# Kernel optimization log

Hardware: AMD Instinct MI355X
Metric: run time of the kernel (lower is better)

The kernel has to match this reference:

```python
import jax, jax.numpy as jnp
import numpy as np

N_NODES = 100000
N_EDGES = 1600000
IN_DIM, HID_DIM, OUT_DIM = 64, 128, 64


def setup_inputs() -> dict:
    key = jax.random.key(0)
    ks = jax.random.split(key, 12)
    s = 0.02
    x = jax.random.normal(ks[0], (N_NODES, IN_DIM), dtype=jnp.float32)
    edge_index = jax.random.randint(ks[1], (2, N_EDGES), 0, N_NODES, dtype=jnp.int64)
    return {
        "x": x,
        "edge_index": edge_index,
        # SAGEConv layer 1: lin_l (neighbors, with bias), lin_r (root, no bias)
        "w1l": jax.random.normal(ks[2], (HID_DIM, IN_DIM), dtype=jnp.float32) * s,
        "b1l": jnp.zeros((HID_DIM,), dtype=jnp.float32),
        "w1r": jax.random.normal(ks[3], (HID_DIM, IN_DIM), dtype=jnp.float32) * s,
        # SAGEConv layer 2
        "w2l": jax.random.normal(ks[4], (OUT_DIM, HID_DIM), dtype=jnp.float32) * s,
        "b2l": jnp.zeros((OUT_DIM,), dtype=jnp.float32),
        "w2r": jax.random.normal(ks[5], (OUT_DIM, HID_DIM), dtype=jnp.float32) * s,
        # classifier MLP: Linear(128,64) -> ReLU -> Linear(64,2) (dropout off in eval)
        "wc1": jax.random.normal(ks[6], (64, 2 * OUT_DIM), dtype=jnp.float32) * s,
        "bc1": jnp.zeros((64,), dtype=jnp.float32),
        "wc2": jax.random.normal(ks[7], (2, 64), dtype=jnp.float32) * s,
        "bc2": jnp.zeros((2,), dtype=jnp.float32),
    }


def _sage_conv(x, src, dst, wl, bl, wr):
    # PyG SAGEConv (aggr='mean'): out = lin_l(mean_{j in N(i)} x_j) + lin_r(x_i)
    msg = x[src]                                                  # [E, d] gather
    agg = jax.ops.segment_sum(msg, dst, num_segments=N_NODES)     # [N, d] scatter-add
    cnt = jax.ops.segment_sum(jnp.ones((src.shape[0],), x.dtype), dst, num_segments=N_NODES)
    mean = agg / jnp.maximum(cnt, 1.0)[:, None]
    return mean @ wl.T + bl + x @ wr.T


def reference(x, edge_index, w1l, b1l, w1r, w2l, b2l, w2r, wc1, bc1, wc2, bc2):
    src, dst = edge_index[0], edge_index[1]
    h = jax.nn.relu(_sage_conv(x, src, dst, w1l, b1l, w1r))   # dropout: eval mode (identity)
    h = jax.nn.relu(_sage_conv(h, src, dst, w2l, b2l, w2r))
    edge_repr = jnp.concatenate([h[src], h[dst]], axis=1)      # [E, 2*OUT_DIM]
    hidden = jax.nn.relu(edge_repr @ wc1.T + bc1)
    return hidden @ wc2.T + bc2                                 # [E, 2]
```

## Files before the change

kernel.cpp:

```cpp
#include <hip/hip_runtime.h>

#define N_NODES 100000
#define N_EDGES 1600000
#define NBLK_SCAN 391
#define SLICE_NODES 12500
#define BCAP 800000

typedef unsigned int uint;
typedef unsigned short ushort;
typedef __attribute__((ext_vector_type(8))) short bf16x8;
typedef __attribute__((ext_vector_type(4))) float f32x4;

__device__ inline float bflo(uint u) { union { uint i; float f; } c; c.i = u << 16; return c.f; }
__device__ inline float bfhi(uint u) { union { uint i; float f; } c; c.i = u & 0xffff0000u; return c.f; }
__device__ inline float bf2f(ushort h) { union { uint i; float f; } c; c.i = (uint)h << 16; return c.f; }
__device__ inline ushort f2bf(float f) {
    union { float f; uint u; } c; c.f = f;
    uint r = (c.u + 0x7fffu + ((c.u >> 16) & 1u)) >> 16;
    return (ushort)r;
}

#define W1_OFF   0
#define W2L_OFF  16384
#define W2R_OFF  24576
#define WC1_OFF  32768
#define W_TOTAL  40960

__global__ __launch_bounds__(256) void prep_weights(const float* __restrict__ w1r,
                                                    const float* __restrict__ w1l,
                                                    const float* __restrict__ w2l,
                                                    const float* __restrict__ w2r,
                                                    const float* __restrict__ wc1,
                                                    ushort* __restrict__ Whi,
                                                    ushort* __restrict__ Wlo) {
    int idx = blockIdx.x * 256 + threadIdx.x;
    if (idx >= W_TOTAL) return;
    float v;
    if (idx < W2L_OFF) {
        int o = idx >> 7, k = idx & 127;
        v = (k < 64) ? w1r[o * 64 + k] : w1l[o * 64 + (k - 64)];
    } else if (idx < W2R_OFF) {
        int t2 = idx - W2L_OFF; int o = t2 >> 7, k = t2 & 127;
        v = w2l[o * 128 + k];
    } else if (idx < WC1_OFF) {
        int t2 = idx - W2R_OFF; int o = t2 >> 7, k = t2 & 127;
        v = w2r[o * 128 + k];
    } else {
        int t2 = idx - WC1_OFF; int o = t2 >> 6, k = t2 & 63;
        v = wc1[(o & 63) * 128 + ((o >> 6) << 6) + k];
    }
    ushort hi = f2bf(v);
    ushort lo = f2bf(v - bf2f(hi));
    Whi[idx] = hi; Wlo[idx] = lo;
}

__global__ __launch_bounds__(256) void convert_kernel(const float* __restrict__ x,
                                                      ushort* __restrict__ xb) {
    int i = blockIdx.x * 256 + threadIdx.x;
    if (i < N_NODES * 32) {
        float2 v = ((const float2*)x)[i];
        uint o = (uint)f2bf(v.x) | ((uint)f2bf(v.y) << 16);
        ((uint*)xb)[i] = o;
    }
}

__global__ __launch_bounds__(256) void bucket_kernel(const int* __restrict__ src,
                                                     const int* __restrict__ dst,
                                                     int* __restrict__ cnt,
                                                     int* __restrict__ bcur,
                                                     uint* __restrict__ bkt) {
    __shared__ int hist[8];
    __shared__ int bbase[8];
    const int t = threadIdx.x;
    int e = blockIdx.x * 256 + t;
    if (t < 8) hist[t] = 0;
    __syncthreads();
    int b = -1, mo = 0; uint pack = 0;
    if (e < N_EDGES) {
        int d = dst[e], s = src[e];
        atomicAdd(&cnt[d], 1);
        b = d / SLICE_NODES;
        pack = ((uint)(d - b * SLICE_NODES) << 17) | (uint)s;
        mo = atomicAdd(&hist[b], 1);
    }
    __syncthreads();
    if (t < 8) bbase[t] = hist[t] ? atomicAdd(&bcur[t], hist[t]) : 0;
    __syncthreads();
    if (b >= 0) {
        int pos = bbase[b] + mo;
        if (pos < BCAP) bkt[(size_t)b * BCAP + pos] = pack;
    }
}

__global__ __launch_bounds__(256) void scan_block_sums(const int* __restrict__ cnt,
                                                       int* __restrict__ partial) {
    __shared__ int red[4];
    int i = blockIdx.x * 256 + threadIdx.x;
    int v = (i < N_NODES) ? cnt[i] : 0;
#pragma unroll
    for (int off = 32; off; off >>= 1) v += __shfl_down(v, off, 64);
    if ((threadIdx.x & 63) == 0) red[threadIdx.x >> 6] = v;
    __syncthreads();
    if (threadIdx.x == 0) partial[blockIdx.x] = red[0] + red[1] + red[2] + red[3];
}

__global__ __launch_bounds__(512) void scan_top(int* __restrict__ partial) {
    __shared__ int s[512];
    int t = threadIdx.x;
    int orig = (t < NBLK_SCAN) ? partial[t] : 0;
    s[t] = orig;
    __syncthreads();
#pragma unroll
    for (int off = 1; off < 512; off <<= 1) {
        int v = (t >= off) ? s[t - off] : 0;
        __syncthreads();
        s[t] += v;
        __syncthreads();
    }
    if (t < NBLK_SCAN) partial[t] = s[t] - orig;
}

__global__ __launch_bounds__(256) void scan_final(const int* __restrict__ cnt,
                                                  const int* __restrict__ partial,
                                                  int* __restrict__ row_start,
                                                  int* __restrict__ cursor) {
    __shared__ int s[256];
    int i = blockIdx.x * 256 + threadIdx.x;
    int t = threadIdx.x;
    int orig = (i < N_NODES) ? cnt[i] : 0;
    s[t] = orig;
    __syncthreads();
#pragma unroll
    for (int off = 1; off < 256; off <<= 1) {
        int v = (t >= off) ? s[t - off] : 0;
        __syncthreads();
        s[t] += v;
        __syncthreads();
    }
    if (i < N_NODES) {
        int rs = partial[blockIdx.x] + s[t] - orig;
        row_start[i] = rs;
        cursor[i] = rs;
    }
}

__global__ __launch_bounds__(256) void fill_bucketed(const uint* __restrict__ bkt,
                                                     const int* __restrict__ bcur,
                                                     int* __restrict__ cursor,
                                                     int* __restrict__ nbr) {
    int slice = blockIdx.x & 7;
    int chunk = blockIdx.x >> 3;
    int count = min(bcur[slice], BCAP);
    int per = (count + 127) >> 7;
    int start = chunk * per;
    int end = min(start + per, count);
    const uint* B = bkt + (size_t)slice * BCAP;
    for (int i = start + threadIdx.x; i < end; i += 256) {
        uint p = B[i];
        int d = slice * SLICE_NODES + (int)(p >> 17);
        int pos = atomicAdd(&cursor[d], 1);
        nbr[pos] = (int)(p & 0x1FFFFu);
    }
}

__global__ __launch_bounds__(256) void agg_mean64_bf16(const int* __restrict__ row_start,
                                                       const int* __restrict__ cnt,
                                                       const int* __restrict__ nbr,
                                                       const ushort* __restrict__ feat,
                                                       float* __restrict__ outmean) {
    int node = blockIdx.x * 4 + (threadIdx.x >> 6);
    if (node >= N_NODES) return;
    int lane = threadIdx.x & 63;
    int half = lane >> 5;
    int f2   = lane & 31;
    int s = row_start[node];
    int d = cnt[node];
    float ax = 0.0f, ay = 0.0f;
    int p = 0;
    for (; p + 4 <= d; p += 4) {
        int n0 = nbr[s + p + half];
        int n1 = nbr[s + p + 2 + half];
        uint w0 = *(const uint*)(feat + (size_t)n0 * 64 + f2 * 2);
        uint w1 = *(const uint*)(feat + (size_t)n1 * 64 + f2 * 2);
        ax += bflo(w0) + bflo(w1);
        ay += bfhi(w0) + bfhi(w1);
    }
    for (; p + 2 <= d; p += 2) {
        int n0 = nbr[s + p + half];
        uint w0 = *(const uint*)(feat + (size_t)n0 * 64 + f2 * 2);
        ax += bflo(w0);
        ay += bfhi(w0);
    }
    if (p < d && half == 0) {
        int n0 = nbr[s + p];
        uint w0 = *(const uint*)(feat + (size_t)n0 * 64 + f2 * 2);
        ax += bflo(w0);
        ay += bfhi(w0);
    }
    ax += __shfl_xor(ax, 32, 64);
    ay += __shfl_xor(ay, 32, 64);
    if (half == 0) {
        float inv = 1.0f / fmaxf((float)d, 1.0f);
        float2 o; o.x = ax * inv; o.y = ay * inv;
        *(float2*)&outmean[(size_t)node * 64 + f2 * 2] = o;
    }
}

#define MFMA __builtin_amdgcn_mfma_f32_16x16x32_bf16

__global__ __launch_bounds__(256) void g1g2_kernel(const float* __restrict__ x,
                                                   const float* __restrict__ mean1,
                                                   const ushort* __restrict__ Whi,
                                                   const ushort* __restrict__ Wlo,
                                                   const float* __restrict__ b1l,
                                                   ushort* __restrict__ h1hi,
                                                   ushort* __restrict__ y2b) {
    __shared__ ushort Ah[64 * 136];
    __shared__ ushort Al[64 * 136];
    const int t = threadIdx.x;
    const int l = t & 63;
    const int wv = t >> 6;
    const int base = blockIdx.x * 64;
    const int lr = l & 15;
    const int lk = (l >> 4) * 8;

    for (int idx = t; idx < 2048; idx += 256) {
        int halfsel = idx >> 10;
        int id2 = idx & 1023;
        int n = id2 >> 4;
        int k0 = (id2 & 15) * 4;
        int gn = base + n;
        float4 v = make_float4(0.f, 0.f, 0.f, 0.f);
        if (gn < N_NODES) v = *(const float4*)&(halfsel ? mean1 : x)[(size_t)gn * 64 + k0];
        ushort h0 = f2bf(v.x), h1_ = f2bf(v.y), h2_ = f2bf(v.z), h3 = f2bf(v.w);
        ushort l0 = f2bf(v.x - bf2f(h0)), l1 = f2bf(v.y - bf2f(h1_));
        ushort l2 = f2bf(v.z - bf2f(h2_)), l3 = f2bf(v.w - bf2f(h3));
        int col = halfsel * 64 + k0;
        uint2 ph; ph.x = (uint)h0 | ((uint)h1_ << 16); ph.y = (uint)h2_ | ((uint)h3 << 16);
        uint2 pl; pl.x = (uint)l0 | ((uint)l1 << 16); pl.y = (uint)l2 | ((uint)l3 << 16);
        *(uint2*)&Ah[n * 136 + col] = ph;
        *(uint2*)&Al[n * 136 + col] = pl;
    }
    __syncthreads();

    f32x4 acc[4][2];
#pragma unroll
    for (int m4 = 0; m4 < 4; ++m4)
#pragma unroll
        for (int n2 = 0; n2 < 2; ++n2) acc[m4][n2] = (f32x4){0.f, 0.f, 0.f, 0.f};

#pragma unroll
    for (int ks = 0; ks < 4; ++ks) {
        bf16x8 ah[4], al[4];
        int aoff = lr * 136 + ks * 32 + lk;
#pragma unroll
        for (int m4 = 0; m4 < 4; ++m4) {
            ah[m4] = *(const bf16x8*)&Ah[m4 * 2176 + aoff];
            al[m4] = *(const bf16x8*)&Al[m4 * 2176 + aoff];
        }
#pragma unroll
        for (int n2 = 0; n2 < 2; ++n2) {
            int o = wv * 32 + n2 * 16 + lr;
            int woff = W1_OFF + o * 128 + ks * 32 + lk;
            bf16x8 bh = *(const bf16x8*)&Whi[woff];
            bf16x8 bl = *(const bf16x8*)&Wlo[woff];
#pragma unroll
            for (int m4 = 0; m4 < 4; ++m4) {
                acc[m4][n2] = MFMA(al[m4], bh, acc[m4][n2], 0, 0, 0);
                acc[m4][n2] = MFMA(ah[m4], bl, acc[m4][n2], 0, 0, 0);
                acc[m4][n2] = MFMA(ah[m4], bh, acc[m4][n2], 0, 0, 0);
            }
        }
    }
    __syncthreads();
    ushort* H1h = Ah;
    ushort* H1l = Al;

#pragma unroll
    for (int n2 = 0; n2 < 2; ++n2) {
        int o = wv * 32 + n2 * 16 + lr;
        float bb = b1l[o];
#pragma unroll
        for (int m4 = 0; m4 < 4; ++m4) {
#pragma unroll
            for (int r = 0; r < 4; ++r) {
                int nl = m4 * 16 + (l >> 4) * 4 + r;
                float val = fmaxf(acc[m4][n2][r] + bb, 0.f);
                ushort hi = f2bf(val);
                ushort lo = f2bf(val - bf2f(hi));
                H1h[nl * 136 + o] = hi;
                H1l[nl * 136 + o] = lo;
            }
        }
    }
    __syncthreads();

    for (int idx = t; idx < 2048; idx += 256) {
        int n = idx >> 5;
        int c4 = (idx & 31) * 4;
        int gn = base + n;
        if (gn < N_NODES)
            *(uint2*)&h1hi[(size_t)gn * 128 + c4] = *(uint2*)&H1h[n * 136 + c4];
    }

    f32x4 acc2[4];
#pragma unroll
    for (int m4 = 0; m4 < 4; ++m4) acc2[m4] = (f32x4){0.f, 0.f, 0.f, 0.f};
#pragma unroll
    for (int ks = 0; ks < 4; ++ks) {
        int aoff = lr * 136 + ks * 32 + lk;
        int o2 = wv * 16 + lr;
        int woff = W2L_OFF + o2 * 128 + ks * 32 + lk;
        bf16x8 bh = *(const bf16x8*)&Whi[woff];
        bf16x8 bl = *(const bf16x8*)&Wlo[woff];
#pragma unroll
        for (int m4 = 0; m4 < 4; ++m4) {
            bf16x8 ah = *(const bf16x8*)&H1h[m4 * 2176 + aoff];
            bf16x8 al = *(const bf16x8*)&H1l[m4 * 2176 + aoff];
            acc2[m4] = MFMA(al, bh, acc2[m4], 0, 0, 0);
            acc2[m4] = MFMA(ah, bl, acc2[m4], 0, 0, 0);
            acc2[m4] = MFMA(ah, bh, acc2[m4], 0, 0, 0);
        }
    }
#pragma unroll
    for (int m4 = 0; m4 < 4; ++m4) {
#pragma unroll
        for (int r = 0; r < 4; ++r) {
            int nl = m4 * 16 + (l >> 4) * 4 + r;
            int gn = base + nl;
            if (gn < N_NODES) y2b[(size_t)gn * 64 + wv * 16 + lr] = f2bf(acc2[m4][r]);
        }
    }
}

__global__ __launch_bounds__(256) void g3g4_kernel(const ushort* __restrict__ h1hi,
                                                   const float* __restrict__ mean2,
                                                   const ushort* __restrict__ Whi,
                                                   const ushort* __restrict__ Wlo,
                                                   const float* __restrict__ b2l,
                                                   const float* __restrict__ bc1,
                                                   ushort* __restrict__ uvb) {
    __shared__ ushort H1h[64 * 136];
    __shared__ float  M2[64 * 68];
    __shared__ ushort H2l[64 * 72];
    const int t = threadIdx.x;
    const int l = t & 63;
    const int wv = t >> 6;
    const int base = blockIdx.x * 64;
    const int lr = l & 15;
    const int lk = (l >> 4) * 8;

    for (int idx = t; idx < 2048; idx += 256) {
        int n = idx >> 5;
        int c4 = (idx & 31) * 4;
        int gn = base + n;
        uint2 vh = make_uint2(0u, 0u);
        if (gn < N_NODES) vh = *(const uint2*)&h1hi[(size_t)gn * 128 + c4];
        *(uint2*)&H1h[n * 136 + c4] = vh;
    }
    for (int idx = t; idx < 1024; idx += 256) {
        int n = idx >> 4;
        int k0 = (idx & 15) * 4;
        int gn = base + n;
        float4 v = make_float4(0.f, 0.f, 0.f, 0.f);
        if (gn < N_NODES) v = *(const float4*)&mean2[(size_t)gn * 64 + k0];
        *(float4*)&M2[n * 68 + k0] = v;
    }
    __syncthreads();

    f32x4 acc[4];
#pragma unroll
    for (int m4 = 0; m4 < 4; ++m4) acc[m4] = (f32x4){0.f, 0.f, 0.f, 0.f};
#pragma unroll
    for (int ks = 0; ks < 4; ++ks) {
        int aoff = lr * 136 + ks * 32 + lk;
        int o2 = wv * 16 + lr;
        int woff = W2R_OFF + o2 * 128 + ks * 32 + lk;
        bf16x8 bh = *(const bf16x8*)&Whi[woff];
        bf16x8 bl = *(const bf16x8*)&Wlo[woff];
#pragma unroll
        for (int m4 = 0; m4 < 4; ++m4) {
            bf16x8 ah = *(const bf16x8*)&H1h[m4 * 2176 + aoff];
            acc[m4] = MFMA(ah, bl, acc[m4], 0, 0, 0);
            acc[m4] = MFMA(ah, bh, acc[m4], 0, 0, 0);
        }
    }
    __syncthreads();
    ushort* H2h = H1h;

    {
        int o2 = wv * 16 + lr;
        float bb = b2l[o2];
#pragma unroll
        for (int m4 = 0; m4 < 4; ++m4) {
#pragma unroll
            for (int r = 0; r < 4; ++r) {
                int nl = m4 * 16 + (l >> 4) * 4 + r;
                float val = fmaxf(acc[m4][r] + M2[nl * 68 + o2] + bb, 0.f);
                ushort hi = f2bf(val);
                ushort lo = f2bf(val - bf2f(hi));
                H2h[nl * 72 + o2] = hi;
                H2l[nl * 72 + o2] = lo;
            }
        }
    }
    __syncthreads();

    f32x4 acc4[4][2];
#pragma unroll
    for (int m4 = 0; m4 < 4; ++m4)
#pragma unroll
        for (int n2 = 0; n2 < 2; ++n2) acc4[m4][n2] = (f32x4){0.f, 0.f, 0.f, 0.f};
#pragma unroll
    for (int ks = 0; ks < 2; ++ks) {
        bf16x8 ah[4], al[4];
        int aoff = lr * 72 + ks * 32 + lk;
#pragma unroll
        for (int m4 = 0; m4 < 4; ++m4) {
            ah[m4] = *(const bf16x8*)&H2h[m4 * 1152 + aoff];
            al[m4] = *(const bf16x8*)&H2l[m4 * 1152 + aoff];
        }
#pragma unroll
        for (int n2 = 0; n2 < 2; ++n2) {
            int o = wv * 32 + n2 * 16 + lr;
            int woff = WC1_OFF + o * 64 + ks * 32 + lk;
            bf16x8 bh = *(const bf16x8*)&Whi[woff];
            bf16x8 bl = *(const bf16x8*)&Wlo[woff];
#pragma unroll
            for (int m4 = 0; m4 < 4; ++m4) {
                acc4[m4][n2] = MFMA(al[m4], bh, acc4[m4][n2], 0, 0, 0);
                acc4[m4][n2] = MFMA(ah[m4], bl, acc4[m4][n2], 0, 0, 0);
                acc4[m4][n2] = MFMA(ah[m4], bh, acc4[m4][n2], 0, 0, 0);
            }
        }
    }
#pragma unroll
    for (int n2 = 0; n2 < 2; ++n2) {
        int o = wv * 32 + n2 * 16 + lr;
        float bb = (o < 64) ? bc1[o] : 0.0f;
#pragma unroll
        for (int m4 = 0; m4 < 4; ++m4) {
#pragma unroll
            for (int r = 0; r < 4; ++r) {
                int nl = m4 * 16 + (l >> 4) * 4 + r;
                int gn = base + nl;
                if (gn < N_NODES) uvb[(size_t)gn * 128 + o] = f2bf(acc4[m4][n2][r] + bb);
            }
        }
    }
}

__global__ __launch_bounds__(256) void edge_kernel(const int* __restrict__ src,
                                                   const int* __restrict__ dst,
                                                   const ushort* __restrict__ uvb,
                                                   const float* __restrict__ wc2,
                                                   const float* __restrict__ bc2,
                                                   float* __restrict__ out) {
    int e = blockIdx.x * blockDim.x + threadIdx.x;
    if (e >= N_EDGES) return;
    const uint4* ua = (const uint4*)(uvb + (size_t)src[e] * 128);
    const uint4* va = (const uint4*)(uvb + (size_t)dst[e] * 128 + 64);
    float o0 = 0.0f, o1 = 0.0f;
#pragma unroll
    for (int k = 0; k < 8; ++k) {
        uint4 a = ua[k], b = va[k];
        int i0 = k * 8;
        float h0, h1v;
        h0 = fmaxf(bflo(a.x) + bflo(b.x), 0.f); h1v = fmaxf(bfhi(a.x) + bfhi(b.x), 0.f);
        o0 += wc2[i0] * h0 + wc2[i0 + 1] * h1v;  o1 += wc2[64 + i0] * h0 + wc2[65 + i0] * h1v;
        h0 = fmaxf(bflo(a.y) + bflo(b.y), 0.f); h1v = fmaxf(bfhi(a.y) + bfhi(b.y), 0.f);
        o0 += wc2[i0 + 2] * h0 + wc2[i0 + 3] * h1v;  o1 += wc2[66 + i0] * h0 + wc2[67 + i0] * h1v;
        h0 = fmaxf(bflo(a.z) + bflo(b.z), 0.f); h1v = fmaxf(bfhi(a.z) + bfhi(b.z), 0.f);
        o0 += wc2[i0 + 4] * h0 + wc2[i0 + 5] * h1v;  o1 += wc2[68 + i0] * h0 + wc2[69 + i0] * h1v;
        h0 = fmaxf(bflo(a.w) + bflo(b.w), 0.f); h1v = fmaxf(bfhi(a.w) + bfhi(b.w), 0.f);
        o0 += wc2[i0 + 6] * h0 + wc2[i0 + 7] * h1v;  o1 += wc2[70 + i0] * h0 + wc2[71 + i0] * h1v;
    }
    float2 r;
    r.x = o0 + bc2[0];
    r.y = o1 + bc2[1];
    *(float2*)(out + (size_t)e * 2) = r;
}

extern "C" void kernel_launch(void* const* d_in, const int* in_sizes, int n_in,
                              void* d_out, int out_size, void* d_ws, size_t ws_size,
                              hipStream_t stream) {
    const float* x   = (const float*)d_in[0];
    const int*   ei  = (const int*)d_in[1];
    const float* w1l = (const float*)d_in[2];
    const float* b1l = (const float*)d_in[3];
    const float* w1r = (const float*)d_in[4];
    const float* w2l = (const float*)d_in[5];
    const float* b2l = (const float*)d_in[6];
    const float* w2r = (const float*)d_in[7];
    const float* wc1 = (const float*)d_in[8];
    const float* bc1 = (const float*)d_in[9];
    const float* wc2 = (const float*)d_in[10];
    const float* bc2 = (const float*)d_in[11];
    float* out = (float*)d_out;

    const int* srcp = ei;
    const int* dstp = ei + N_EDGES;

    float*  ws    = (float*)d_ws;
    ushort* xb    = (ushort*)ws;
    ushort* y2b   = (ushort*)ws;
    float*  mean1 = ws + 3200000;
    ushort* uvb   = (ushort*)(ws + 3200000);
    ushort* h1hi  = (ushort*)(ws + 9600000);
    uint*   bkt   = (uint*)(ws + 16000000);
    float*  mean2 = ws + 22400000;
    int*    ib    = (int*)(ws + 28800000);
    int* cnt       = ib;
    int* row_start = ib + 100000;
    int* cursor    = ib + 200000;
    int* partial   = ib + 300000;
    int* bcur      = ib + 300512;
    int* nbr       = ib + 300520;
    ushort* Whi = (ushort*)(ws + 30800000);
    ushort* Wlo = (ushort*)(ws + 30900000);

    hipMemsetAsync(cnt, 0, (size_t)N_NODES * 4, stream);
    hipMemsetAsync(bcur, 0, 8 * 4, stream);

    prep_weights<<<(W_TOTAL + 255) / 256, 256, 0, stream>>>(w1r, w1l, w2l, w2r, wc1, Whi, Wlo);
    convert_kernel<<<12500, 256, 0, stream>>>(x, xb);

    bucket_kernel<<<(N_EDGES + 255) / 256, 256, 0, stream>>>(srcp, dstp, cnt, bcur, bkt);
    scan_block_sums<<<NBLK_SCAN, 256, 0, stream>>>(cnt, partial);
    scan_top<<<1, 512, 0, stream>>>(partial);
    scan_final<<<NBLK_SCAN, 256, 0, stream>>>(cnt, partial, row_start, cursor);
    fill_bucketed<<<1024, 256, 0, stream>>>(bkt, bcur, cursor, nbr);

    const int NAB = (N_NODES + 3) / 4;
    const int NB  = (N_NODES + 63) / 64;

    agg_mean64_bf16<<<NAB, 256, 0, stream>>>(row_start, cnt, nbr, xb, mean1);
    g1g2_kernel<<<NB, 256, 0, stream>>>(x, mean1, Whi, Wlo, b1l, h1hi, y2b);
    agg_mean64_bf16<<<NAB, 256, 0, stream>>>(row_start, cnt, nbr, y2b, mean2);
    g3g4_kernel<<<NB, 256, 0, stream>>>(h1hi, mean2, Whi, Wlo, b2l, bc1, uvb);
    edge_kernel<<<(N_EDGES + 255) / 256, 256, 0, stream>>>(srcp, dstp, uvb, wc2, bc2, out);
}
```

Measured before the change: 470.9 us.

## Split bucket counters into 64 groups and process 2048 edges per block

The bucketing kernel now gives each block 2048 edges instead of 256. It counts slice histograms in a first pass and scatters in a second pass. Blocks are spread over 8 groups of bucket counters (64 counters in total), which cuts global-atomic contention on the 8 shared bucket cursors. The fill kernel is reorganised to walk the 64 sub-buckets. The cost is that dst is read twice and each sub-bucket has a cap of 100000, which the uniform random input should stay under.

```diff
diff --git a/kernel.cpp b/kernel.cpp
--- a/kernel.cpp
+++ b/kernel.cpp
@@ -4,7 +4,9 @@
 #define N_EDGES 1600000
 #define NBLK_SCAN 391
 #define SLICE_NODES 12500
-#define BCAP 800000
+#define BCAP 100000
+#define EPB 2048
+#define NBLK_BKT 782
 
 typedef unsigned int uint;
 typedef unsigned short ushort;
@@ -69,26 +71,28 @@
                                                      int* __restrict__ cnt,
                                                      int* __restrict__ bcur,
                                                      uint* __restrict__ bkt) {
-    __shared__ int hist[8];
-    __shared__ int bbase[8];
+    __shared__ int hist[8], hist2[8], bbase[8];
     const int t = threadIdx.x;
-    int e = blockIdx.x * 256 + t;
-    if (t < 8) hist[t] = 0;
-    __syncthreads();
-    int b = -1, mo = 0; uint pack = 0;
-    if (e < N_EDGES) {
+    const int g = blockIdx.x & 7;
+    const int ebase = blockIdx.x * EPB;
+    const int eend = min(ebase + EPB, N_EDGES);
+    if (t < 8) { hist[t] = 0; hist2[t] = 0; }
+    __syncthreads();
+    for (int e = ebase + t; e < eend; e += 256) {
+        int d = dst[e];
+        atomicAdd(&cnt[d], 1);
+        atomicAdd(&hist[d / SLICE_NODES], 1);
+    }
+    __syncthreads();
+    if (t < 8) bbase[t] = hist[t] ? atomicAdd(&bcur[g * 8 + t], hist[t]) : 0;
+    __syncthreads();
+    for (int e = ebase + t; e < eend; e += 256) {
         int d = dst[e], s = src[e];
-        atomicAdd(&cnt[d], 1);
-        b = d / SLICE_NODES;
-        pack = ((uint)(d - b * SLICE_NODES) << 17) | (uint)s;
-        mo = atomicAdd(&hist[b], 1);
-    }
-    __syncthreads();
-    if (t < 8) bbase[t] = hist[t] ? atomicAdd(&bcur[t], hist[t]) : 0;
-    __syncthreads();
-    if (b >= 0) {
+        int b = d / SLICE_NODES;
+        uint pack = ((uint)(d - b * SLICE_NODES) << 17) | (uint)s;
+        int mo = atomicAdd(&hist2[b], 1);
         int pos = bbase[b] + mo;
-        if (pos < BCAP) bkt[(size_t)b * BCAP + pos] = pack;
+        if (pos < BCAP) bkt[(size_t)(g * 8 + b) * BCAP + pos] = pack;
     }
 }
 
@@ -148,16 +152,17 @@
                                                      const int* __restrict__ bcur,
                                                      int* __restrict__ cursor,
                                                      int* __restrict__ nbr) {
-    int slice = blockIdx.x & 7;
-    int chunk = blockIdx.x >> 3;
-    int count = min(bcur[slice], BCAP);
-    int per = (count + 127) >> 7;
+    int s = blockIdx.x & 7;
+    int g = (blockIdx.x >> 3) & 7;
+    int chunk = blockIdx.x >> 6;
+    int count = min(bcur[g * 8 + s], BCAP);
+    int per = (count + 15) >> 4;
     int start = chunk * per;
     int end = min(start + per, count);
-    const uint* B = bkt + (size_t)slice * BCAP;
+    const uint* B = bkt + (size_t)(g * 8 + s) * BCAP;
     for (int i = start + threadIdx.x; i < end; i += 256) {
         uint p = B[i];
-        int d = slice * SLICE_NODES + (int)(p >> 17);
+        int d = s * SLICE_NODES + (int)(p >> 17);
         int pos = atomicAdd(&cursor[d], 1);
         nbr[pos] = (int)(p & 0x1FFFFu);
     }
@@ -515,17 +520,17 @@
     int* cursor    = ib + 200000;
     int* partial   = ib + 300000;
     int* bcur      = ib + 300512;
-    int* nbr       = ib + 300520;
+    int* nbr       = ib + 300576;
     ushort* Whi = (ushort*)(ws + 30800000);
     ushort* Wlo = (ushort*)(ws + 30900000);
 
     hipMemsetAsync(cnt, 0, (size_t)N_NODES * 4, stream);
-    hipMemsetAsync(bcur, 0, 8 * 4, stream);
+    hipMemsetAsync(bcur, 0, 64 * 4, stream);
 
     prep_weights<<<(W_TOTAL + 255) / 256, 256, 0, stream>>>(w1r, w1l, w2l, w2r, wc1, Whi, Wlo);
     convert_kernel<<<12500, 256, 0, stream>>>(x, xb);
 
-    bucket_kernel<<<(N_EDGES + 255) / 256, 256, 0, stream>>>(srcp, dstp, cnt, bcur, bkt);
+    bucket_kernel<<<NBLK_BKT, 256, 0, stream>>>(srcp, dstp, cnt, bcur, bkt);
     scan_block_sums<<<NBLK_SCAN, 256, 0, stream>>>(cnt, partial);
     scan_top<<<1, 512, 0, stream>>>(partial);
     scan_final<<<NBLK_SCAN, 256, 0, stream>>>(cnt, partial, row_start, cursor);
```

Measured after the change: 448.5 us. 4.8% less time.
